# Optimization experiments

Hardware: AMD Instinct MI355X
Metric: run time of the kernel (lower is better)

Reference implementation:

```python
import jax, jax.numpy as jnp
import numpy as np

EMBED = 1024
HEADS = 16
HEAD_DIM = EMBED // HEADS


def setup_inputs() -> dict:
    key = jax.random.key(0)
    ks = jax.random.split(key, 12)
    B, S = 2, 2048
    inp = {
        "query": jax.random.normal(ks[0], (B, S, EMBED), dtype=jnp.float32),
        "key": jax.random.normal(ks[1], (B, S, EMBED), dtype=jnp.float32),
        "value": jax.random.normal(ks[2], (B, S, EMBED), dtype=jnp.float32),
        "mask": jnp.ones((B, 1, 1, S), dtype=jnp.int32),
    }
    scale = 1.0 / np.sqrt(EMBED)
    inp["Wq"] = jax.random.normal(ks[3], (EMBED, EMBED), dtype=jnp.float32) * scale
    inp["bq"] = jax.random.normal(ks[4], (EMBED,), dtype=jnp.float32) * 0.01
    inp["Wk"] = jax.random.normal(ks[5], (EMBED, EMBED), dtype=jnp.float32) * scale
    inp["bk"] = jax.random.normal(ks[6], (EMBED,), dtype=jnp.float32) * 0.01
    inp["Wv"] = jax.random.normal(ks[7], (EMBED, EMBED), dtype=jnp.float32) * scale
    inp["bv"] = jax.random.normal(ks[8], (EMBED,), dtype=jnp.float32) * 0.01
    inp["Wo"] = jax.random.normal(ks[9], (EMBED, EMBED), dtype=jnp.float32) * scale
    inp["bo"] = jax.random.normal(ks[10], (EMBED,), dtype=jnp.float32) * 0.01
    return inp


def reference(query, key, value, mask, Wq, bq, Wk, bk, Wv, bv, Wo, bo):
    N, Lq, _ = query.shape
    Lk = key.shape[1]
    # Linear projections (torch Linear: x @ W.T + b)
    q = (query @ Wq.T + bq).reshape(N, Lq, HEADS, HEAD_DIM)
    k = (key @ Wk.T + bk).reshape(N, Lk, HEADS, HEAD_DIM)
    v = (value @ Wv.T + bv).reshape(N, Lk, HEADS, HEAD_DIM)
    # scores: [N, H, Lq, Lk]
    energy = jnp.einsum("nqhd,nkhd->nhqk", q, k)
    energy = jnp.where(mask == 0, jnp.float32(-1e20), energy)
    # NOTE: original scales by sqrt(embedSize), not sqrt(head_dim)
    attn = jax.nn.softmax(energy / jnp.sqrt(jnp.float32(EMBED)), axis=3)
    out = jnp.einsum("nhqv,nvhd->nqhd", attn, v).reshape(N, Lq, EMBED)
    return out @ Wo.T + bo
```

## Files before the change

### kernel.cpp

```cpp
#include <hip/hip_runtime.h>
#include <stdint.h>

typedef unsigned short u16;
typedef __attribute__((ext_vector_type(8))) short short8;
typedef __attribute__((ext_vector_type(4))) short short4v;
typedef __attribute__((ext_vector_type(4))) float floatx4;
typedef __attribute__((ext_vector_type(2))) unsigned int uint2v;
typedef __attribute__((ext_vector_type(4))) unsigned int uint4v;

#define AS_GLOBAL __attribute__((address_space(1)))
#define AS_LDS    __attribute__((address_space(3)))

#define QSCALE 0.045084220f

__device__ __forceinline__ float bf2f(u16 u) {
  union { unsigned int i; float f; } x; x.i = ((unsigned int)u) << 16; return x.f;
}
__device__ __forceinline__ u16 f2bf(float f) {
  union { float f; unsigned int i; } x; x.f = f;
  unsigned int u = x.i;
  u += 0x7fffu + ((u >> 16) & 1u);
  return (u16)(u >> 16);
}
__device__ __forceinline__ u16 f2bf_fast(float f) {
  union { float f; unsigned int i; } x; x.f = f;
  return (u16)((x.i + 0x8000u) >> 16);
}

__device__ __forceinline__ unsigned int cvtpk_bf16(float lo, float hi) {
  unsigned int w;
  __asm__("v_cvt_pk_bf16_f32 %0, %1, %2" : "=v"(w) : "v"(lo), "v"(hi));
  return w;
}

__device__ __forceinline__ void pl32_swap(unsigned int& a, unsigned int& b) {
#if __has_builtin(__builtin_amdgcn_permlane32_swap)
  uint2v r = __builtin_amdgcn_permlane32_swap(a, b, false, false);
  a = r[0]; b = r[1];
#else
  __asm__("v_permlane32_swap_b32 %0, %1" : "+v"(a), "+v"(b));
#endif
}
__device__ __forceinline__ void pl16_swap(unsigned int& a, unsigned int& b) {
#if __has_builtin(__builtin_amdgcn_permlane16_swap)
  uint2v r = __builtin_amdgcn_permlane16_swap(a, b, false, false);
  a = r[0]; b = r[1];
#else
  __asm__("v_permlane16_swap_b32 %0, %1" : "+v"(a), "+v"(b));
#endif
}

__device__ __forceinline__ int probe_is_f32(const void* p) {
  const unsigned int* w = (const unsigned int*)p;
  int cnt = 0;
#pragma unroll
  for (int i = 0; i < 64; ++i) {
    unsigned int lo = w[i] & 0xFFFFu;
    int e = (int)((lo >> 7) & 0xFFu);
    cnt += (e >= 117 && e <= 137) ? 1 : 0;
  }
  return cnt < 32;
}

__device__ __forceinline__ short8 ld8(const void* P, size_t off, int isf32) {
  if (isf32) {
    const float* q = (const float*)P + off;
    float4 x = *(const float4*)q;
    float4 y = *(const float4*)(q + 4);
    short8 r;
    r[0] = (short)f2bf(x.x); r[1] = (short)f2bf(x.y);
    r[2] = (short)f2bf(x.z); r[3] = (short)f2bf(x.w);
    r[4] = (short)f2bf(y.x); r[5] = (short)f2bf(y.y);
    r[6] = (short)f2bf(y.z); r[7] = (short)f2bf(y.w);
    return r;
  }
  return *(const short8*)((const u16*)P + off);
}

__device__ __forceinline__ float ldscalar(const void* P, size_t idx, int isf32) {
  return isf32 ? ((const float*)P)[idx] : bf2f(((const u16*)P)[idx]);
}

__global__ __launch_bounds__(256) void cvt7(
    const void* s0, const void* s1, const void* s2, const void* s3,
    const void* s4, const void* s5, const void* s6,
    u16* d0, u16* d1, u16* d2, u16* d3, u16* d4, u16* d5, u16* d6)
{
  const int z = blockIdx.y;
  const void* src; u16* dst; int n;
  switch (z) {
    case 0: src = s0; dst = d0; n = 4194304; break;
    case 1: src = s1; dst = d1; n = 4194304; break;
    case 2: src = s2; dst = d2; n = 4194304; break;
    case 3: src = s3; dst = d3; n = 1048576; break;
    case 4: src = s4; dst = d4; n = 1048576; break;
    case 5: src = s5; dst = d5; n = 1048576; break;
    default: src = s6; dst = d6; n = 1048576; break;
  }
  const int isf32 = probe_is_f32(src);
  for (int i = blockIdx.x * 256 + threadIdx.x; i * 4 < n; i += gridDim.x * 256) {
    if (isf32) {
      float4 x = ((const float4*)src)[i];
      short4v r;
      r[0] = (short)f2bf(x.x); r[1] = (short)f2bf(x.y);
      r[2] = (short)f2bf(x.z); r[3] = (short)f2bf(x.w);
      *(short4v*)(dst + (size_t)i * 4) = r;
    } else {
      *(short4v*)(dst + (size_t)i * 4) = ((const short4v*)src)[i];
    }
  }
}

__device__ __forceinline__ void gemm_core_bf16(
    const u16* __restrict__ A, const u16* __restrict__ W,
    u16* As, u16* Bs, floatx4 acc[4][4], int m0, int n0, int K, int tid)
{
  const int lane = tid & 63, wv = tid >> 6;
  const int wm = wv >> 1, wn = wv & 1;
  const int g = lane >> 4, ml = lane & 15;
  const int r0 = tid >> 2, kc = (tid & 3) << 3;
  const u16* Ag0 = A + (size_t)(m0 + r0) * K + kc;
  const u16* Ag1 = A + (size_t)(m0 + r0 + 64) * K + kc;
  const u16* Bg0 = W + (size_t)(n0 + r0) * K + kc;
  const u16* Bg1 = W + (size_t)(n0 + r0 + 64) * K + kc;

#define STAGE_QKV(buf_, kt_) do {                                              \
    u16* a0 = As + (buf_) * 4096 + tid * 8;                                    \
    u16* b0 = Bs + (buf_) * 4096 + tid * 8;                                    \
    __builtin_amdgcn_global_load_lds((const AS_GLOBAL unsigned int*)(Ag0 + (kt_)), \
                                     (AS_LDS unsigned int*)a0, 16, 0, 0);      \
    __builtin_amdgcn_global_load_lds((const AS_GLOBAL unsigned int*)(Ag1 + (kt_)), \
                                     (AS_LDS unsigned int*)(a0 + 2048), 16, 0, 0); \
    __builtin_amdgcn_global_load_lds((const AS_GLOBAL unsigned int*)(Bg0 + (kt_)), \
                                     (AS_LDS unsigned int*)b0, 16, 0, 0);      \
    __builtin_amdgcn_global_load_lds((const AS_GLOBAL unsigned int*)(Bg1 + (kt_)), \
                                     (AS_LDS unsigned int*)(b0 + 2048), 16, 0, 0); \
  } while (0)

  STAGE_QKV(0, 0);
  int buf = 0;
#pragma unroll 2
  for (int kt = 0; kt < K; kt += 32) {
    const int nk = (kt + 32 < K) ? (kt + 32) : 0;
    STAGE_QKV(buf ^ 1, nk);
    __asm__ __volatile__("s_waitcnt vmcnt(4)\n\ts_barrier" ::: "memory");
    const u16* Ac = As + buf * 4096;
    const u16* Bc = Bs + buf * 4096;
    short8 af[4], bf[4];
#pragma unroll
    for (int i = 0; i < 4; ++i)
      af[i] = *(const short8*)(Ac + (wm * 64 + i * 16 + ml) * 32 + g * 8);
#pragma unroll
    for (int j = 0; j < 4; ++j)
      bf[j] = *(const short8*)(Bc + (wn * 64 + j * 16 + ml) * 32 + g * 8);
#pragma unroll
    for (int i = 0; i < 4; ++i)
#pragma unroll
      for (int j = 0; j < 4; ++j)
        acc[i][j] = __builtin_amdgcn_mfma_f32_16x16x32_bf16(af[i], bf[j], acc[i][j], 0, 0, 0);
    __asm__ __volatile__("s_waitcnt lgkmcnt(0)\n\ts_barrier" ::: "memory");
    buf ^= 1;
  }
#undef STAGE_QKV
  __asm__ __volatile__("s_waitcnt vmcnt(0)" ::: "memory");
}

__device__ __forceinline__ void gemm_core_cvt(
    const void* __restrict__ A, const void* __restrict__ W, int aF32, int bF32,
    u16* As, u16* Bs, floatx4 acc[4][4], int m0, int n0, int K, int tid)
{
  const int lane = tid & 63, wv = tid >> 6;
  const int wm = wv >> 1, wn = wv & 1;
  const int g = lane >> 4, ml = lane & 15;
  const int r0 = tid >> 2, kc = (tid & 3) << 3;
  const size_t offA0 = (size_t)(m0 + r0) * K + kc;
  const size_t offA1 = (size_t)(m0 + r0 + 64) * K + kc;
  const size_t offB0 = (size_t)(n0 + r0) * K + kc;
  const size_t offB1 = (size_t)(n0 + r0 + 64) * K + kc;
  u16* Al0 = As + tid * 8;  u16* Al1 = As + (tid + 256) * 8;
  u16* Bl0 = Bs + tid * 8;  u16* Bl1 = Bs + (tid + 256) * 8;
  for (int kt = 0; kt < K; kt += 32) {
    short8 a0 = ld8(A, offA0 + kt, aF32);
    short8 a1 = ld8(A, offA1 + kt, aF32);
    short8 b0 = ld8(W, offB0 + kt, bF32);
    short8 b1 = ld8(W, offB1 + kt, bF32);
    *(short8*)Al0 = a0;  *(short8*)Al1 = a1;
    *(short8*)Bl0 = b0;  *(short8*)Bl1 = b1;
    __syncthreads();
    short8 af[4], bf[4];
#pragma unroll
    for (int i = 0; i < 4; ++i)
      af[i] = *(const short8*)(As + (wm * 64 + i * 16 + ml) * 32 + g * 8);
#pragma unroll
    for (int j = 0; j < 4; ++j)
      bf[j] = *(const short8*)(Bs + (wn * 64 + j * 16 + ml) * 32 + g * 8);
#pragma unroll
    for (int i = 0; i < 4; ++i)
#pragma unroll
      for (int j = 0; j < 4; ++j)
        acc[i][j] = __builtin_amdgcn_mfma_f32_16x16x32_bf16(af[i], bf[j], acc[i][j], 0, 0, 0);
    __syncthreads();
  }
}

__device__ __forceinline__ void qkv_epilogue(
    floatx4 acc[4][4], const void* Bi, int cF32, u16* O, int m0, int n0,
    int tid, int z)
{
  const int lane = tid & 63, wv = tid >> 6;
  const int wm = wv >> 1, wn = wv & 1, g = lane >> 4, ml = lane & 15;
  const float sc = (z == 0) ? QSCALE : 1.0f;
#pragma unroll
  for (int j = 0; j < 4; ++j) {
    int gn = n0 + wn * 64 + j * 16 + ml;
    float bvv = ldscalar(Bi, (size_t)gn, cF32);
    int h = gn >> 6, d = gn & 63;
    if (z == 2) {
#pragma unroll
      for (int i = 0; i < 4; ++i) {
        int gm0 = m0 + wm * 64 + i * 16 + g * 4;
        int b = gm0 >> 11, s0 = gm0 & 2047;
        short4v pk;
#pragma unroll
        for (int r = 0; r < 4; ++r) pk[r] = (short)f2bf_fast(acc[i][j][r] + bvv);
        *(short4v*)(O + ((((size_t)b * 16 + h) * 64 + d) * 2048 + s0)) = pk;
      }
    } else {
#pragma unroll
      for (int i = 0; i < 4; ++i)
#pragma unroll
        for (int r = 0; r < 4; ++r) {
          int gm = m0 + wm * 64 + i * 16 + g * 4 + r;
          int b = gm >> 11, s = gm & 2047;
          O[(((size_t)b * 16 + h) * 2048 + s) * 64 + d] =
              f2bf_fast((acc[i][j][r] + bvv) * sc);
        }
    }
  }
}

__global__ __launch_bounds__(256) void qkv_gemm_bf16(
    const u16* __restrict__ Xq, const u16* __restrict__ Xk, const u16* __restrict__ Xv,
    const u16* __restrict__ Wq, const u16* __restrict__ Wk, const u16* __restrict__ Wv,
    const void* __restrict__ Bq, const void* __restrict__ Bk, const void* __restrict__ Bv,
    u16* __restrict__ Oq, u16* __restrict__ Ok, u16* __restrict__ Ov)
{
  __align__(16) __shared__ u16 As[8192];
  __align__(16) __shared__ u16 Bs[8192];
  const int z = blockIdx.z;
  const u16* X = (z == 0) ? Xq : (z == 1) ? Xk : Xv;
  const u16* W = (z == 0) ? Wq : (z == 1) ? Wk : Wv;
  const void* Bi = (z == 0) ? Bq : (z == 1) ? Bk : Bv;
  u16* O = (z == 0) ? Oq : (z == 1) ? Ok : Ov;
  const int tid = threadIdx.x;
  const int m0 = blockIdx.x * 128, n0 = blockIdx.y * 128;
  floatx4 acc[4][4] = {};
  gemm_core_bf16(X, W, As, Bs, acc, m0, n0, 1024, tid);
  const int cF32 = probe_is_f32(Bi);
  qkv_epilogue(acc, Bi, cF32, O, m0, n0, tid, z);
}

__global__ __launch_bounds__(256) void qkv_gemm_cvt(
    const void* __restrict__ Xq, const void* __restrict__ Xk, const void* __restrict__ Xv,
    const void* __restrict__ Wq, const void* __restrict__ Wk, const void* __restrict__ Wv,
    const void* __restrict__ Bq, const void* __restrict__ Bk, const void* __restrict__ Bv,
    u16* __restrict__ Oq, u16* __restrict__ Ok, u16* __restrict__ Ov)
{
  __align__(16) __shared__ u16 As[4096];
  __align__(16) __shared__ u16 Bs[4096];
  const int z = blockIdx.z;
  const void* X  = (z == 0) ? Xq : (z == 1) ? Xk : Xv;
  const void* W  = (z == 0) ? Wq : (z == 1) ? Wk : Wv;
  const void* Bi = (z == 0) ? Bq : (z == 1) ? Bk : Bv;
  u16* O = (z == 0) ? Oq : (z == 1) ? Ok : Ov;
  const int aF32 = probe_is_f32(X);
  const int bF32 = probe_is_f32(W);
  const int cF32 = probe_is_f32(Bi);
  const int tid = threadIdx.x;
  const int m0 = blockIdx.y * 128, n0 = blockIdx.x * 128;
  floatx4 acc[4][4] = {};
  gemm_core_cvt(X, W, aF32, bF32, As, Bs, acc, m0, n0, 1024, tid);
  qkv_epilogue(acc, Bi, cF32, O, m0, n0, tid, z);
}

__global__ __launch_bounds__(256) void out_gemm_bf16(
    const u16* __restrict__ X, const u16* __restrict__ W,
    const void* __restrict__ Bi, float* __restrict__ O)
{
  __align__(16) __shared__ u16 As[8192];
  __align__(16) __shared__ u16 Bs[8192];
  const int tid = threadIdx.x;
  const int m0 = blockIdx.x * 128, n0 = blockIdx.y * 128;
  floatx4 acc[4][4] = {};
  gemm_core_bf16(X, W, As, Bs, acc, m0, n0, 1024, tid);
  const int cF32 = probe_is_f32(Bi);
  const int lane = tid & 63, wv = tid >> 6;
  const int wm = wv >> 1, wn = wv & 1, g = lane >> 4, ml = lane & 15;
#pragma unroll
  for (int j = 0; j < 4; ++j) {
    int gn = n0 + wn * 64 + j * 16 + ml;
    float bvv = ldscalar(Bi, (size_t)gn, cF32);
#pragma unroll
    for (int i = 0; i < 4; ++i)
#pragma unroll
      for (int r = 0; r < 4; ++r) {
        int gm = m0 + wm * 64 + i * 16 + g * 4 + r;
        O[(size_t)gm * 1024 + gn] = acc[i][j][r] + bvv;
      }
  }
}

__global__ __launch_bounds__(256) void out_gemm_cvt(
    const u16* __restrict__ X, const void* __restrict__ W,
    const void* __restrict__ Bi, float* __restrict__ O)
{
  __align__(16) __shared__ u16 As[4096];
  __align__(16) __shared__ u16 Bs[4096];
  const int bF32 = probe_is_f32(W);
  const int cF32 = probe_is_f32(Bi);
  const int tid = threadIdx.x;
  const int m0 = blockIdx.y * 128, n0 = blockIdx.x * 128;
  floatx4 acc[4][4] = {};
  gemm_core_cvt(X, W, 0, bF32, As, Bs, acc, m0, n0, 1024, tid);
  const int lane = tid & 63, wv = tid >> 6;
  const int wm = wv >> 1, wn = wv & 1, g = lane >> 4, ml = lane & 15;
#pragma unroll
  for (int j = 0; j < 4; ++j) {
    int gn = n0 + wn * 64 + j * 16 + ml;
    float bvv = ldscalar(Bi, (size_t)gn, cF32);
#pragma unroll
    for (int i = 0; i < 4; ++i)
#pragma unroll
      for (int r = 0; r < 4; ++r) {
        int gm = m0 + wm * 64 + i * 16 + g * 4 + r;
        O[(size_t)gm * 1024 + gn] = acc[i][j][r] + bvv;
      }
  }
}

__global__ __launch_bounds__(256) void flash_attn(
    const u16* __restrict__ Q, const u16* __restrict__ K, const u16* __restrict__ V,
    const int* __restrict__ Mask, u16* __restrict__ O)
{
  __align__(16) __shared__ u16 Ks[2][64 * 64];
  __align__(16) __shared__ u16 Vt[64 * 64];
  __align__(16) __shared__ int Ms[64];
  __shared__ int Wok[4];

  const int qt = blockIdx.x;
  const int bh = blockIdx.y;
  const int b = bh >> 4, h = bh & 15;
  const int tid = threadIdx.x;
  const int lane = tid & 63, wv = tid >> 6;
  const int g = lane >> 4, ml = lane & 15;

  const size_t baseQ  = (((size_t)b * 16 + h) * 2048 + (size_t)qt * 64) * 64;
  const size_t baseKV = ((size_t)b * 16 + h) * 2048 * 64;

  {
    int la = 1;
#pragma unroll
    for (int i = 0; i < 8; ++i) la &= Mask[b * 2048 + tid * 8 + i];
    int wall = __all(la != 0);
    if (lane == 0) Wok[wv] = wall;
  }

  short8 qf[2];
#pragma unroll
  for (int ks = 0; ks < 2; ++ks)
    qf[ks] = *(const short8*)(Q + baseQ + (size_t)(wv * 16 + ml) * 64 + ks * 32 + g * 8);

  const u16* kg[2]; const u16* vg[2];
  int lo[2];
#pragma unroll
  for (int t = 0; t < 2; ++t) {
    int s = tid + t * 256;
    int krow = s >> 3, kch = (s & 7) ^ (krow & 7);
    kg[t] = K + baseKV + (size_t)krow * 64 + kch * 8;
    int vd = s >> 3,  vch = (s & 7) ^ (vd & 7);
    vg[t] = V + baseKV + (size_t)vd * 2048 + vch * 8;
    lo[t] = ((tid & 448) + t * 256) * 8;
  }

#pragma unroll
  for (int t = 0; t < 2; ++t)
    __builtin_amdgcn_global_load_lds((const AS_GLOBAL unsigned int*)kg[t],
                                     (AS_LDS unsigned int*)(&Ks[0][0] + lo[t]), 16, 0, 0);

  __syncthreads();
  const bool maskall = Wok[0] && Wok[1] && Wok[2] && Wok[3];

  floatx4 oacc[4] = {};
  float lp = 0.f;

  int buf = 0;
#pragma unroll 2
  for (int kv0 = 0; kv0 < 2048; kv0 += 64) {
#pragma unroll
    for (int t = 0; t < 2; ++t)
      __builtin_amdgcn_global_load_lds((const AS_GLOBAL unsigned int*)(vg[t] + kv0),
                                       (AS_LDS unsigned int*)(Vt + lo[t]), 16, 0, 0);
    const int nxt = (kv0 + 64) & 2047;
#pragma unroll
    for (int t = 0; t < 2; ++t)
      __builtin_amdgcn_global_load_lds((const AS_GLOBAL unsigned int*)(kg[t] + (size_t)nxt * 64),
                                       (AS_LDS unsigned int*)(&Ks[buf ^ 1][0] + lo[t]), 16, 0, 0);
    if (!maskall && tid < 64) Ms[tid] = Mask[b * 2048 + kv0 + tid];
    __asm__ __volatile__("s_waitcnt vmcnt(4) lgkmcnt(0)\n\ts_barrier" ::: "memory");

    const u16* Kc = &Ks[buf][0];
    float sv[4][4];
    __builtin_amdgcn_s_setprio(1);
#pragma unroll
    for (int j = 0; j < 4; ++j) {
      floatx4 a = {0.f, 0.f, 0.f, 0.f};
      int row = j * 16 + ml;
#pragma unroll
      for (int ks = 0; ks < 2; ++ks) {
        short8 kb = *(const short8*)(Kc + row * 64 + ((((ks << 2) + g) ^ (row & 7)) << 3));
        a = __builtin_amdgcn_mfma_f32_16x16x32_bf16(kb, qf[ks], a, 0, 0, 0);
      }
#pragma unroll
      for (int r = 0; r < 4; ++r) sv[j][r] = a[r];
    }
    __builtin_amdgcn_s_setprio(0);
    if (!maskall) {
#pragma unroll
      for (int j = 0; j < 4; ++j)
#pragma unroll
        for (int r = 0; r < 4; ++r)
          if (Ms[j * 16 + g * 4 + r] == 0) sv[j][r] = -1.0e30f;
    }

#pragma unroll
    for (int j = 0; j < 4; ++j)
#pragma unroll
      for (int r = 0; r < 4; ++r) {
        float p = __builtin_amdgcn_exp2f(sv[j][r]);
        sv[j][r] = p;
        lp += p;
      }

    unsigned int Wd[4][2];
#pragma unroll
    for (int j = 0; j < 4; ++j)
#pragma unroll
      for (int w = 0; w < 2; ++w)
        Wd[j][w] = cvtpk_bf16(sv[j][2 * w], sv[j][2 * w + 1]);

    unsigned int Zl[2][2], Zh[2][2];
#pragma unroll
    for (int jd = 0; jd < 2; ++jd)
#pragma unroll
      for (int w = 0; w < 2; ++w) {
        unsigned int ua = Wd[2 * jd][w];
        unsigned int ub = Wd[2 * jd + 1][w];
        pl32_swap(ua, ub);
        pl16_swap(ua, ub);
        Zl[jd][w] = ua;
        Zh[jd][w] = ub;
      }

    short8 pa[2];
#pragma unroll
    for (int ks = 0; ks < 2; ++ks) {
      uint4v pw;
      pw[0] = Zl[ks][0]; pw[1] = Zl[ks][1];
      pw[2] = Zh[ks][0]; pw[3] = Zh[ks][1];
      pa[ks] = __builtin_bit_cast(short8, pw);
    }

    __asm__ __volatile__("s_waitcnt vmcnt(2)\n\ts_barrier" ::: "memory");

    __builtin_amdgcn_s_setprio(1);
#pragma unroll
    for (int t = 0; t < 4; ++t)
#pragma unroll
      for (int j2 = 0; j2 < 2; ++j2) {
        short8 vb = *(const short8*)(Vt + (t * 16 + ml) * 64 + ((((j2 << 2) + g) ^ (ml & 7)) << 3));
        oacc[t] = __builtin_amdgcn_mfma_f32_16x16x32_bf16(pa[j2], vb, oacc[t], 0, 0, 0);
      }
    __builtin_amdgcn_s_setprio(0);

    __asm__ __volatile__("s_barrier" ::: "memory");
    buf ^= 1;
  }
  __asm__ __volatile__("s_waitcnt vmcnt(0)" ::: "memory");

  float l = lp;
  l += __shfl_xor(l, 16);
  l += __shfl_xor(l, 32);
  float inv[4];
#pragma unroll
  for (int r = 0; r < 4; ++r) {
    float lr = __shfl(l, (lane & 48) | (((lane >> 4) & 3) * 4 + r));
    inv[r] = (lr > 0.f) ? 1.0f / lr : 0.f;
  }
#pragma unroll
  for (int t = 0; t < 4; ++t)
#pragma unroll
    for (int r = 0; r < 4; ++r) {
      int q = qt * 64 + wv * 16 + g * 4 + r;
      int d = t * 16 + ml;
      O[((size_t)b * 2048 + q) * 1024 + h * 64 + d] = f2bf_fast(oacc[t][r] * inv[r]);
    }
}

extern "C" void kernel_launch(void* const* d_in, const int* in_sizes, int n_in,
                              void* d_out, int out_size, void* d_ws, size_t ws_size,
                              hipStream_t stream) {
  const void* q_in = d_in[0];
  const void* k_in = d_in[1];
  const void* v_in = d_in[2];
  const int* mask = (const int*)d_in[3];
  const void* Wq = d_in[4];  const void* bq = d_in[5];
  const void* Wk = d_in[6];  const void* bk = d_in[7];
  const void* Wv = d_in[8];  const void* bv = d_in[9];
  const void* Wo = d_in[10]; const void* bo = d_in[11];

  const size_t NTOK = (size_t)2 * 2048 * 1024;
  const size_t NW   = (size_t)1024 * 1024;

  if (ws_size >= (size_t)67108864) {
    u16* CXq = (u16*)d_ws;
    u16* CXk = CXq + NTOK;
    u16* CXv = CXk + NTOK;
    u16* CWq = CXv + NTOK;
    u16* CWk = CWq + NW;
    u16* CWv = CWk + NW;
    u16* CWo = CWv + NW;
    u16* Qp  = CWo + NW;
    u16* Kp  = Qp + NTOK;
    u16* Vp  = Kp + NTOK;
    u16* Ao  = Vp + NTOK;

    cvt7<<<dim3(1024, 7), 256, 0, stream>>>(q_in, k_in, v_in, Wq, Wk, Wv, Wo,
                                            CXq, CXk, CXv, CWq, CWk, CWv, CWo);
    qkv_gemm_bf16<<<dim3(32, 8, 3), 256, 0, stream>>>(CXq, CXk, CXv,
                                                      CWq, CWk, CWv,
                                                      bq, bk, bv, Qp, Kp, Vp);
    flash_attn<<<dim3(32, 32), 256, 0, stream>>>(Qp, Kp, Vp, mask, Ao);
    out_gemm_bf16<<<dim3(32, 8), 256, 0, stream>>>(Ao, CWo, bo, (float*)d_out);
  } else {
    u16* Qp = (u16*)d_ws;
    u16* Kp = Qp + NTOK;
    u16* Vp = Kp + NTOK;
    u16* Ao = Vp + NTOK;

    qkv_gemm_cvt<<<dim3(8, 32, 3), 256, 0, stream>>>(q_in, k_in, v_in,
                                                     Wq, Wk, Wv, bq, bk, bv,
                                                     Qp, Kp, Vp);
    flash_attn<<<dim3(32, 32), 256, 0, stream>>>(Qp, Kp, Vp, mask, Ao);
    out_gemm_cvt<<<dim3(8, 32), 256, 0, stream>>>(Ao, Wo, bo, (float*)d_out);
  }
}
```

Before: 250.0 us.

## Switch flash attention to 32x32x16 MFMA with two-wave blocks

The attention kernel now uses 32x32x16 bf16 MFMA tiles instead of 16x16x32, with each wave owning 32 query rows, and blocks shrink from four waves to two. The softmax probability repacking needs only permlane32 swaps, and K/V tile staging is spread over more loads per thread. This cuts MFMA instruction count and the shuffle overhead per tile. In exchange each block has fewer waves to hide latency, and the larger accumulators raise register pressure.

```diff
diff --git a/kernel.cpp b/kernel.cpp
--- a/kernel.cpp
+++ b/kernel.cpp
@@ -5,6 +5,7 @@
 typedef __attribute__((ext_vector_type(8))) short short8;
 typedef __attribute__((ext_vector_type(4))) short short4v;
 typedef __attribute__((ext_vector_type(4))) float floatx4;
+typedef __attribute__((ext_vector_type(16))) float floatx16;
 typedef __attribute__((ext_vector_type(2))) unsigned int uint2v;
 typedef __attribute__((ext_vector_type(4))) unsigned int uint4v;
 
@@ -39,14 +40,6 @@
   a = r[0]; b = r[1];
 #else
   __asm__("v_permlane32_swap_b32 %0, %1" : "+v"(a), "+v"(b));
-#endif
-}
-__device__ __forceinline__ void pl16_swap(unsigned int& a, unsigned int& b) {
-#if __has_builtin(__builtin_amdgcn_permlane16_swap)
-  uint2v r = __builtin_amdgcn_permlane16_swap(a, b, false, false);
-  a = r[0]; b = r[1];
-#else
-  __asm__("v_permlane16_swap_b32 %0, %1" : "+v"(a), "+v"(b));
 #endif
 }
 
@@ -338,21 +331,21 @@
   }
 }
 
-__global__ __launch_bounds__(256) void flash_attn(
+__global__ __launch_bounds__(128) void flash_attn(
     const u16* __restrict__ Q, const u16* __restrict__ K, const u16* __restrict__ V,
     const int* __restrict__ Mask, u16* __restrict__ O)
 {
   __align__(16) __shared__ u16 Ks[2][64 * 64];
   __align__(16) __shared__ u16 Vt[64 * 64];
   __align__(16) __shared__ int Ms[64];
-  __shared__ int Wok[4];
+  __shared__ int Wok[2];
 
   const int qt = blockIdx.x;
   const int bh = blockIdx.y;
   const int b = bh >> 4, h = bh & 15;
   const int tid = threadIdx.x;
   const int lane = tid & 63, wv = tid >> 6;
-  const int g = lane >> 4, ml = lane & 15;
+  const int H = lane >> 5, lq = lane & 31;
 
   const size_t baseQ  = (((size_t)b * 16 + h) * 2048 + (size_t)qt * 64) * 64;
   const size_t baseKV = ((size_t)b * 16 + h) * 2048 * 64;
@@ -360,126 +353,125 @@
   {
     int la = 1;
 #pragma unroll
-    for (int i = 0; i < 8; ++i) la &= Mask[b * 2048 + tid * 8 + i];
+    for (int i = 0; i < 16; ++i) la &= Mask[b * 2048 + tid * 16 + i];
     int wall = __all(la != 0);
     if (lane == 0) Wok[wv] = wall;
   }
 
-  short8 qf[2];
-#pragma unroll
-  for (int ks = 0; ks < 2; ++ks)
-    qf[ks] = *(const short8*)(Q + baseQ + (size_t)(wv * 16 + ml) * 64 + ks * 32 + g * 8);
-
-  const u16* kg[2]; const u16* vg[2];
-  int lo[2];
-#pragma unroll
-  for (int t = 0; t < 2; ++t) {
-    int s = tid + t * 256;
-    int krow = s >> 3, kch = (s & 7) ^ (krow & 7);
-    kg[t] = K + baseKV + (size_t)krow * 64 + kch * 8;
-    int vd = s >> 3,  vch = (s & 7) ^ (vd & 7);
-    vg[t] = V + baseKV + (size_t)vd * 2048 + vch * 8;
-    lo[t] = ((tid & 448) + t * 256) * 8;
-  }
-
-#pragma unroll
-  for (int t = 0; t < 2; ++t)
+  short8 qf[4];
+  {
+    const u16* qb = Q + baseQ + (size_t)(wv * 32 + lq) * 64 + H * 8;
+#pragma unroll
+    for (int c = 0; c < 4; ++c)
+      qf[c] = *(const short8*)(qb + c * 16);
+  }
+
+  const u16* kg[4]; const u16* vg[4];
+  int lo[4];
+#pragma unroll
+  for (int t = 0; t < 4; ++t) {
+    int s = tid + t * 128;
+    int row = s >> 3, ch = (s & 7) ^ (row & 7);
+    kg[t] = K + baseKV + (size_t)row * 64 + ch * 8;
+    vg[t] = V + baseKV + (size_t)row * 2048 + ch * 8;
+    lo[t] = ((tid & 64) + t * 128) * 8;
+  }
+
+#pragma unroll
+  for (int t = 0; t < 4; ++t)
     __builtin_amdgcn_global_load_lds((const AS_GLOBAL unsigned int*)kg[t],
                                      (AS_LDS unsigned int*)(&Ks[0][0] + lo[t]), 16, 0, 0);
 
   __syncthreads();
-  const bool maskall = Wok[0] && Wok[1] && Wok[2] && Wok[3];
-
-  floatx4 oacc[4] = {};
+  const bool maskall = Wok[0] && Wok[1];
+
+  floatx16 oacc0 = {}, oacc1 = {};
   float lp = 0.f;
 
   int buf = 0;
 #pragma unroll 2
   for (int kv0 = 0; kv0 < 2048; kv0 += 64) {
 #pragma unroll
-    for (int t = 0; t < 2; ++t)
+    for (int t = 0; t < 4; ++t)
       __builtin_amdgcn_global_load_lds((const AS_GLOBAL unsigned int*)(vg[t] + kv0),
                                        (AS_LDS unsigned int*)(Vt + lo[t]), 16, 0, 0);
     const int nxt = (kv0 + 64) & 2047;
 #pragma unroll
-    for (int t = 0; t < 2; ++t)
+    for (int t = 0; t < 4; ++t)
       __builtin_amdgcn_global_load_lds((const AS_GLOBAL unsigned int*)(kg[t] + (size_t)nxt * 64),
                                        (AS_LDS unsigned int*)(&Ks[buf ^ 1][0] + lo[t]), 16, 0, 0);
     if (!maskall && tid < 64) Ms[tid] = Mask[b * 2048 + kv0 + tid];
-    __asm__ __volatile__("s_waitcnt vmcnt(4) lgkmcnt(0)\n\ts_barrier" ::: "memory");
+    __asm__ __volatile__("s_waitcnt vmcnt(8) lgkmcnt(0)\n\ts_barrier" ::: "memory");
 
     const u16* Kc = &Ks[buf][0];
-    float sv[4][4];
+    floatx16 a0 = {}, a1 = {};
     __builtin_amdgcn_s_setprio(1);
 #pragma unroll
-    for (int j = 0; j < 4; ++j) {
-      floatx4 a = {0.f, 0.f, 0.f, 0.f};
-      int row = j * 16 + ml;
-#pragma unroll
-      for (int ks = 0; ks < 2; ++ks) {
-        short8 kb = *(const short8*)(Kc + row * 64 + ((((ks << 2) + g) ^ (row & 7)) << 3));
-        a = __builtin_amdgcn_mfma_f32_16x16x32_bf16(kb, qf[ks], a, 0, 0, 0);
+    for (int c = 0; c < 4; ++c) {
+      short8 kb = *(const short8*)(Kc + lq * 64 + (((2 * c + H) ^ (lq & 7)) << 3));
+      a0 = __builtin_amdgcn_mfma_f32_32x32x16_bf16(kb, qf[c], a0, 0, 0, 0);
+    }
+#pragma unroll
+    for (int c = 0; c < 4; ++c) {
+      int rr = 32 + lq;
+      short8 kb = *(const short8*)(Kc + rr * 64 + (((2 * c + H) ^ (lq & 7)) << 3));
+      a1 = __builtin_amdgcn_mfma_f32_32x32x16_bf16(kb, qf[c], a1, 0, 0, 0);
+    }
+    __builtin_amdgcn_s_setprio(0);
+
+    float sv0[16], sv1[16];
+#pragma unroll
+    for (int r = 0; r < 16; ++r) { sv0[r] = a0[r]; sv1[r] = a1[r]; }
+    if (!maskall) {
+#pragma unroll
+      for (int r = 0; r < 16; ++r) {
+        int ko = (r & 3) + 8 * (r >> 2) + 4 * H;
+        if (Ms[ko] == 0)      sv0[r] = -1.0e30f;
+        if (Ms[32 + ko] == 0) sv1[r] = -1.0e30f;
       }
-#pragma unroll
-      for (int r = 0; r < 4; ++r) sv[j][r] = a[r];
-    }
-    __builtin_amdgcn_s_setprio(0);
-    if (!maskall) {
-#pragma unroll
-      for (int j = 0; j < 4; ++j)
-#pragma unroll
-        for (int r = 0; r < 4; ++r)
-          if (Ms[j * 16 + g * 4 + r] == 0) sv[j][r] = -1.0e30f;
-    }
-
-#pragma unroll
-    for (int j = 0; j < 4; ++j)
-#pragma unroll
-      for (int r = 0; r < 4; ++r) {
-        float p = __builtin_amdgcn_exp2f(sv[j][r]);
-        sv[j][r] = p;
-        lp += p;
-      }
-
-    unsigned int Wd[4][2];
-#pragma unroll
-    for (int j = 0; j < 4; ++j)
-#pragma unroll
-      for (int w = 0; w < 2; ++w)
-        Wd[j][w] = cvtpk_bf16(sv[j][2 * w], sv[j][2 * w + 1]);
-
-    unsigned int Zl[2][2], Zh[2][2];
-#pragma unroll
-    for (int jd = 0; jd < 2; ++jd)
-#pragma unroll
-      for (int w = 0; w < 2; ++w) {
-        unsigned int ua = Wd[2 * jd][w];
-        unsigned int ub = Wd[2 * jd + 1][w];
-        pl32_swap(ua, ub);
-        pl16_swap(ua, ub);
-        Zl[jd][w] = ua;
-        Zh[jd][w] = ub;
-      }
-
-    short8 pa[2];
-#pragma unroll
-    for (int ks = 0; ks < 2; ++ks) {
-      uint4v pw;
-      pw[0] = Zl[ks][0]; pw[1] = Zl[ks][1];
-      pw[2] = Zh[ks][0]; pw[3] = Zh[ks][1];
-      pa[ks] = __builtin_bit_cast(short8, pw);
-    }
-
-    __asm__ __volatile__("s_waitcnt vmcnt(2)\n\ts_barrier" ::: "memory");
+    }
+#pragma unroll
+    for (int r = 0; r < 16; ++r) {
+      float p0 = __builtin_amdgcn_exp2f(sv0[r]);
+      float p1 = __builtin_amdgcn_exp2f(sv1[r]);
+      sv0[r] = p0; sv1[r] = p1;
+      lp += p0 + p1;
+    }
+
+    unsigned int Wd0[8], Wd1[8];
+#pragma unroll
+    for (int i = 0; i < 8; ++i) {
+      Wd0[i] = cvtpk_bf16(sv0[2 * i], sv0[2 * i + 1]);
+      Wd1[i] = cvtpk_bf16(sv1[2 * i], sv1[2 * i + 1]);
+    }
+    short8 pa[4];
+#define MAKE_PA(dst_, Wsrc_, base_) do {                                       \
+    unsigned int u0 = Wsrc_[base_],     u1 = Wsrc_[(base_) + 1];               \
+    unsigned int v0 = Wsrc_[(base_) + 2], v1 = Wsrc_[(base_) + 3];             \
+    pl32_swap(u0, v0); pl32_swap(u1, v1);                                      \
+    uint4v pw; pw[0] = u0; pw[1] = u1; pw[2] = v0; pw[3] = v1;                 \
+    dst_ = __builtin_bit_cast(short8, pw);                                     \
+  } while (0)
+    MAKE_PA(pa[0], Wd0, 0);
+    MAKE_PA(pa[1], Wd0, 4);
+    MAKE_PA(pa[2], Wd1, 0);
+    MAKE_PA(pa[3], Wd1, 4);
+#undef MAKE_PA
+
+    __asm__ __volatile__("s_waitcnt vmcnt(4)\n\ts_barrier" ::: "memory");
 
     __builtin_amdgcn_s_setprio(1);
 #pragma unroll
-    for (int t = 0; t < 4; ++t)
-#pragma unroll
-      for (int j2 = 0; j2 < 2; ++j2) {
-        short8 vb = *(const short8*)(Vt + (t * 16 + ml) * 64 + ((((j2 << 2) + g) ^ (ml & 7)) << 3));
-        oacc[t] = __builtin_amdgcn_mfma_f32_16x16x32_bf16(pa[j2], vb, oacc[t], 0, 0, 0);
-      }
+    for (int c = 0; c < 4; ++c) {
+      short8 vb = *(const short8*)(Vt + lq * 64 + (((2 * c + H) ^ (lq & 7)) << 3));
+      oacc0 = __builtin_amdgcn_mfma_f32_32x32x16_bf16(pa[c], vb, oacc0, 0, 0, 0);
+    }
+#pragma unroll
+    for (int c = 0; c < 4; ++c) {
+      int rr = 32 + lq;
+      short8 vb = *(const short8*)(Vt + rr * 64 + (((2 * c + H) ^ (lq & 7)) << 3));
+      oacc1 = __builtin_amdgcn_mfma_f32_32x32x16_bf16(pa[c], vb, oacc1, 0, 0, 0);
+    }
     __builtin_amdgcn_s_setprio(0);
 
     __asm__ __volatile__("s_barrier" ::: "memory");
@@ -487,23 +479,18 @@
   }
   __asm__ __volatile__("s_waitcnt vmcnt(0)" ::: "memory");
 
-  float l = lp;
-  l += __shfl_xor(l, 16);
-  l += __shfl_xor(l, 32);
-  float inv[4];
-#pragma unroll
-  for (int r = 0; r < 4; ++r) {
-    float lr = __shfl(l, (lane & 48) | (((lane >> 4) & 3) * 4 + r));
-    inv[r] = (lr > 0.f) ? 1.0f / lr : 0.f;
-  }
-#pragma unroll
-  for (int t = 0; t < 4; ++t)
-#pragma unroll
-    for (int r = 0; r < 4; ++r) {
-      int q = qt * 64 + wv * 16 + g * 4 + r;
-      int d = t * 16 + ml;
-      O[((size_t)b * 2048 + q) * 1024 + h * 64 + d] = f2bf_fast(oacc[t][r] * inv[r]);
-    }
+  float l = lp + __shfl_xor(lp, 32);
+  float inv = (l > 0.f) ? 1.0f / l : 0.f;
+
+#pragma unroll
+  for (int r = 0; r < 16; ++r) {
+    int qo = (r & 3) + 8 * (r >> 2) + 4 * H;
+    float ivr = __shfl(inv, qo);
+    int q = qt * 64 + wv * 32 + qo;
+    size_t orow = ((size_t)b * 2048 + q) * 1024 + (size_t)h * 64;
+    O[orow + lq]      = f2bf_fast(oacc0[r] * ivr);
+    O[orow + 32 + lq] = f2bf_fast(oacc1[r] * ivr);
+  }
 }
 
 extern "C" void kernel_launch(void* const* d_in, const int* in_sizes, int n_in,
@@ -539,18 +526,18 @@
     qkv_gemm_bf16<<<dim3(32, 8, 3), 256, 0, stream>>>(CXq, CXk, CXv,
                                                       CWq, CWk, CWv,
                                                       bq, bk, bv, Qp, Kp, Vp);
-    flash_attn<<<dim3(32, 32), 256, 0, stream>>>(Qp, Kp, Vp, mask, Ao);
+    flash_attn<<<dim3(32, 32), 128, 0, stream>>>(Qp, Kp, Vp, mask, Ao);
     out_gemm_bf16<<<dim3(32, 8), 256, 0, stream>>>(Ao, CWo, bo, (float*)d_out);
   } else {
     u16* Qp = (u16*)d_ws;
     u16* Kp = Qp + NTOK;
     u16* Vp = Kp + NTOK;
-    u16* Ao = Vp + NTOK;
+    u16* Ao  = Vp + NTOK;
 
     qkv_gemm_cvt<<<dim3(8, 32, 3), 256, 0, stream>>>(q_in, k_in, v_in,
                                                      Wq, Wk, Wv, bq, bk, bv,
                                                      Qp, Kp, Vp);
-    flash_attn<<<dim3(32, 32), 256, 0, stream>>>(Qp, Kp, Vp, mask, Ao);
+    flash_attn<<<dim3(32, 32), 128, 0, stream>>>(Qp, Kp, Vp, mask, Ao);
     out_gemm_cvt<<<dim3(8, 32), 256, 0, stream>>>(Ao, Wo, bo, (float*)d_out);
   }
 }
```

Result: no change. 248.0 us (-0.8%).
